# Kernel optimization log

Hardware: AMD Instinct MI355X
Metric: run time of the kernel (lower is better)

The kernel has to match this reference:

```python
import jax, jax.numpy as jnp
import numpy as np

B, S, E, H = 2, 2048, 1024, 16
DK = E // H


def setup_inputs() -> dict:
    key = jax.random.key(0)
    ks = jax.random.split(key, 8)
    scale = 1.0 / np.sqrt(E)
    inp = {
        "query": jax.random.normal(ks[0], (B, S, E), jnp.float32),
        "key": jax.random.normal(ks[1], (B, S, E), jnp.float32),
        "value": jax.random.normal(ks[2], (B, S, E), jnp.float32),
        # causal mask: True = masked out (upper triangle)
        "attn_mask": jnp.triu(jnp.ones((S, S), jnp.bool_), k=1),
        "Wq": jax.random.normal(ks[3], (E, E), jnp.float32) * scale,
        "bq": jnp.zeros((E,), jnp.float32),
        "Wk": jax.random.normal(ks[4], (E, E), jnp.float32) * scale,
        "bk": jnp.zeros((E,), jnp.float32),
        "Wv": jax.random.normal(ks[5], (E, E), jnp.float32) * scale,
        "bv": jnp.zeros((E,), jnp.float32),
        "Wo": jax.random.normal(ks[6], (E, E), jnp.float32) * scale,
        "bo": jnp.zeros((E,), jnp.float32),
    }
    return inp


def reference(query, key, value, attn_mask, Wq, bq, Wk, bk, Wv, bv, Wo, bo):
    bs = query.shape[0]
    # QKV projections, split heads: [B,S,E] -> [B,H,S,DK]
    def proj(x, W, b):
        y = jnp.einsum('bse,ef->bsf', x, W) + b
        return y.reshape(bs, -1, H, DK).transpose(0, 2, 1, 3)

    q = proj(query, Wq, bq)
    k = proj(key, Wk, bk)
    v = proj(value, Wv, bv)

    # scaled dot-product attention with additive -1e9 mask fill
    scores = jnp.einsum('bhqd,bhkd->bhqk', q, k) / np.sqrt(DK).astype(jnp.float32)
    scores = jnp.where(attn_mask[None, None, :, :], jnp.float32(-1e9), scores)
    attn = jax.nn.softmax(scores, axis=-1)
    ctx = jnp.einsum('bhqk,bhkd->bhqd', attn, v)  # [B,H,S,DK]

    concat = ctx.transpose(0, 2, 1, 3).reshape(bs, -1, E)  # [B,S,E]
    return jnp.einsum('bse,ef->bsf', concat, Wo) + bo
```

## Files before the change

kernel.cpp:

```cpp
#include <hip/hip_runtime.h>
#include <hip/hip_bf16.h>

typedef __attribute__((ext_vector_type(8))) short bf16x8;
typedef __attribute__((ext_vector_type(4))) float f32x4;

constexpr int Bc = 2, Sc = 2048, Ec = 1024, Hc = 16, DKc = 64;

__device__ __forceinline__ unsigned short f2b(float f) {
    union { float f; unsigned u; } v; v.f = f;
    unsigned u = v.u;
    return (unsigned short)((u + 0x7FFFu + ((u >> 16) & 1u)) >> 16);
}
__device__ __forceinline__ unsigned short f2bn(float f) {
    return __bfloat16_as_ushort(__float2bfloat16(f));
}
__device__ __forceinline__ float b2f(unsigned short h) {
    union { unsigned u; float f; } v; v.u = ((unsigned)h) << 16;
    return v.f;
}

#define GLOAD16(ldsp, gp)                                                                  \
    __builtin_amdgcn_global_load_lds((const __attribute__((address_space(1))) void*)(gp),  \
                                     (__attribute__((address_space(3))) void*)(ldsp),      \
                                     16, 0, 0)

#define ASM_VM4 asm volatile("s_waitcnt vmcnt(4)" ::: "memory")
#define ASM_VM0 asm volatile("s_waitcnt vmcnt(0)" ::: "memory")
#define ASM_LG0 asm volatile("s_waitcnt lgkmcnt(0)" ::: "memory")
#define ASM_BAR asm volatile("s_barrier" ::: "memory")

__global__ __launch_bounds__(256) void conv_x(
    const float* __restrict__ Xq, const float* __restrict__ Xk, const float* __restrict__ Xv,
    unsigned short* __restrict__ Xb)
{
    const int z = blockIdx.y;
    const float* X = (z == 0) ? Xq : (z == 1) ? Xk : Xv;
    unsigned short* O = Xb + (size_t)z * 4194304;
    const int n4 = 4194304 / 4;
    for (int i = blockIdx.x * 256 + threadIdx.x; i < n4; i += gridDim.x * 256) {
        float4 v = ((const float4*)X)[i];
        ushort4 h; h.x = f2b(v.x); h.y = f2b(v.y); h.z = f2b(v.z); h.w = f2b(v.w);
        ((ushort4*)O)[i] = h;
    }
}

__global__ __launch_bounds__(256) void conv_w(
    const float* __restrict__ Wq, const float* __restrict__ Wk,
    const float* __restrict__ Wv, const float* __restrict__ Wo,
    unsigned short* __restrict__ Wt)
{
    const int z = blockIdx.z;
    const float* W = (z == 0) ? Wq : (z == 1) ? Wk : (z == 2) ? Wv : Wo;
    unsigned short* O = Wt + (size_t)z * 1048576;
    __shared__ unsigned short T[64][65];
    const int k0 = blockIdx.y * 64, n0 = blockIdx.x * 64;
    const int tx = threadIdx.x & 15, ty = threadIdx.x >> 4;
    #pragma unroll
    for (int p = 0; p < 4; p++) {
        float4 v = *(const float4*)&W[(size_t)(k0 + ty + 16 * p) * 1024 + n0 + 4 * tx];
        T[ty + 16 * p][4 * tx + 0] = f2b(v.x);
        T[ty + 16 * p][4 * tx + 1] = f2b(v.y);
        T[ty + 16 * p][4 * tx + 2] = f2b(v.z);
        T[ty + 16 * p][4 * tx + 3] = f2b(v.w);
    }
    __syncthreads();
    #pragma unroll
    for (int p = 0; p < 4; p++) {
        ushort4 o;
        o.x = T[4 * tx + 0][ty + 16 * p];
        o.y = T[4 * tx + 1][ty + 16 * p];
        o.z = T[4 * tx + 2][ty + 16 * p];
        o.w = T[4 * tx + 3][ty + 16 * p];
        *(ushort4*)&O[(size_t)(n0 + ty + 16 * p) * 1024 + k0 + 4 * tx] = o;
    }
}

__global__ __launch_bounds__(512, 2) void gemm_qkv(
    const unsigned short* __restrict__ Xb, const unsigned short* __restrict__ Wt,
    const float* __restrict__ bq, const float* __restrict__ bk, const float* __restrict__ bv,
    unsigned short* __restrict__ Qw, unsigned short* __restrict__ Kw,
    unsigned short* __restrict__ Vt)
{
    const int wgid = blockIdx.x;
    const int xcd = wgid & 7;
    const int s = wgid >> 3;
    const int z = s >> 3;
    const int t8 = s & 7;
    const int nb = t8 >> 1;
    const int mb = (t8 & 1) * 8 + xcd;

    const unsigned short* Ag = Xb + (size_t)z * 4194304;
    const unsigned short* Bg = Wt + (size_t)z * 1048576;
    const float* bias = (z == 0) ? bq : (z == 1) ? bk : bv;

    __shared__ __align__(16) unsigned short SMEM[32768];

    const int tid = threadIdx.x;
    const int m0 = mb * 256, n0 = nb * 256;
    const int lane = tid & 63, c = lane & 15, g = lane >> 4;
    const int w = tid >> 6;
    const int wr = w >> 2;
    const int wc = w & 3;
    const int lcs = ((lane & 3) ^ ((lane >> 3) & 3)) * 8;
    const int rowin = (lane >> 2);

#define QKV_STAGE(buf, kk)                                                                 \
    _Pragma("unroll")                                                                      \
    for (int r2 = 0; r2 < 2; r2++) {                                                       \
        GLOAD16((char*)SMEM + (buf) * 16384 + r2 * 8192 + w * 1024,                        \
                Ag + (size_t)(m0 + r2 * 128 + w * 16 + rowin) * 1024 + (kk) + lcs);        \
        GLOAD16((char*)SMEM + 32768 + (buf) * 16384 + r2 * 8192 + w * 1024,                \
                Bg + (size_t)(n0 + r2 * 128 + w * 16 + rowin) * 1024 + (kk) + lcs);        \
    }

    f32x4 acc[8][4] = {};
    QKV_STAGE(0, 0)
    QKV_STAGE(1, 32)
    for (int t = 0; t < 32; t++) {
        const int cur = t & 1;
        if (t < 31) { ASM_VM4; } else { ASM_VM0; }
        ASM_BAR;
        bf16x8 a[8], b[4];
        const int rchk = (g ^ ((c >> 1) & 3)) << 4;
        #pragma unroll
        for (int m = 0; m < 8; m++)
            a[m] = *(const bf16x8*)((const char*)SMEM + cur * 16384 +
                                    (wr * 128 + m * 16 + c) * 64 + rchk);
        #pragma unroll
        for (int n = 0; n < 4; n++)
            b[n] = *(const bf16x8*)((const char*)SMEM + 32768 + cur * 16384 +
                                    (wc * 64 + n * 16 + c) * 64 + rchk);
        ASM_LG0;
        ASM_BAR;
        if (t + 2 < 32) { QKV_STAGE(cur, (t + 2) * 32) }
        __builtin_amdgcn_s_setprio(1);
        #pragma unroll
        for (int m = 0; m < 8; m++)
            #pragma unroll
            for (int n = 0; n < 4; n++)
                acc[m][n] = __builtin_amdgcn_mfma_f32_16x16x32_bf16(a[m], b[n], acc[m][n], 0, 0, 0);
        __builtin_amdgcn_s_setprio(0);
    }
#undef QKV_STAGE

    if (z == 2) {
        unsigned short* Tr = SMEM;
        #pragma unroll
        for (int p = 0; p < 2; p++) {
            ASM_BAR;
            if ((wc >> 1) == p) {
                #pragma unroll
                for (int n = 0; n < 4; n++) {
                    const int dl = (wc & 1) * 64 + n * 16 + c;
                    const float bv_ = bias[n0 + p * 128 + dl];
                    #pragma unroll
                    for (int m = 0; m < 8; m++) {
                        const int sl = wr * 128 + m * 16 + 4 * g;
                        ushort4 pw;
                        pw.x = f2bn(acc[m][n][0] + bv_);
                        pw.y = f2bn(acc[m][n][1] + bv_);
                        pw.z = f2bn(acc[m][n][2] + bv_);
                        pw.w = f2bn(acc[m][n][3] + bv_);
                        const int sc = (sl >> 2) ^ (dl & 7);
                        *(ushort4*)&Tr[dl * 256 + sc * 4] = pw;
                    }
                }
            }
            ASM_BAR;
            #pragma unroll
            for (int it = 0; it < 16; it++) {
                const int idx = it * 512 + tid;
                const int dl = idx >> 6;
                const int sc0 = idx & 63;
                const int sc = sc0 ^ (dl & 7);
                const ushort4 pw = *(const ushort4*)&Tr[dl * 256 + sc * 4];
                const int gn = n0 + p * 128 + dl;
                const int h = gn >> 6, d = gn & 63;
                const int gm = m0 + sc0 * 4;
                const int bb = gm >> 11, ss = gm & 2047;
                *(ushort4*)&Vt[((size_t)(bb * Hc + h) * DKc + d) * Sc + ss] = pw;
            }
        }
    } else {
        #pragma unroll
        for (int n = 0; n < 4; n++) {
            const int gn = n0 + wc * 64 + n * 16 + c;
            const float bv_ = bias[gn];
            const int h = gn >> 6, d = gn & 63;
            #pragma unroll
            for (int m = 0; m < 8; m++) {
                #pragma unroll
                for (int r = 0; r < 4; r++) {
                    const int gm = m0 + wr * 128 + m * 16 + 4 * g + r;
                    const int bb = gm >> 11, ss = gm & 2047;
                    const float val = acc[m][n][r] + bv_;
                    if (z == 0)
                        Qw[((size_t)(bb * Hc + h) * Sc + ss) * DKc + d] = f2bn(val * 0.125f);
                    else
                        Kw[((size_t)(bb * Hc + h) * Sc + ss) * DKc + d] = f2bn(val);
                }
            }
        }
    }
}

__global__ __launch_bounds__(256) void gemm_out(
    const unsigned short* __restrict__ Ctx, const unsigned short* __restrict__ Wt,
    const float* __restrict__ bo, float* __restrict__ Out)
{
    const int wgid = blockIdx.x;
    const int xcd = wgid & 7, slot = wgid >> 3;
    const int y = xcd + 8 * (slot & 3);
    const int x = slot >> 2;

    const unsigned short* Ag = Ctx;
    const unsigned short* Bg = Wt + (size_t)3 * 1048576;

    __shared__ __align__(16) unsigned short SMEM[4][4096];

    const int tid = threadIdx.x;
    const int m0 = y * 128, n0 = x * 128;
    const int lane = tid & 63, c = lane & 15, g = lane >> 4;
    const int w = tid >> 6;
    const int wr = (w >> 1) * 64, wc = (w & 1) * 64;
    const int lr = lane >> 2;
    const int lcs = ((lane & 3) ^ ((lane >> 3) & 3)) * 8;

#define OUT_STAGE(buf, kk)                                                                 \
    _Pragma("unroll")                                                                      \
    for (int i = 0; i < 2; i++) {                                                          \
        const int rb = 32 * w + 16 * i;                                                    \
        GLOAD16(SMEM[buf] + rb * 32, Ag + (size_t)(m0 + rb + lr) * 1024 + (kk) + lcs);     \
        GLOAD16(SMEM[2 + (buf)] + rb * 32, Bg + (size_t)(n0 + rb + lr) * 1024 + (kk) + lcs); \
    }

    f32x4 acc[4][4] = {};
    OUT_STAGE(0, 0)
    OUT_STAGE(1, 32)
    for (int t = 0; t < 32; t++) {
        const int cur = t & 1;
        if (t < 31) { ASM_VM4; } else { ASM_VM0; }
        ASM_BAR;
        bf16x8 a[4], b[4];
        #pragma unroll
        for (int m = 0; m < 4; m++)
            a[m] = *(const bf16x8*)((const char*)SMEM[cur] +
                   (wr + 16 * m + c) * 64 + ((g ^ ((c >> 1) & 3)) << 4));
        #pragma unroll
        for (int n = 0; n < 4; n++)
            b[n] = *(const bf16x8*)((const char*)SMEM[2 + cur] +
                   (wc + 16 * n + c) * 64 + ((g ^ ((c >> 1) & 3)) << 4));
        ASM_LG0;
        ASM_BAR;
        if (t + 2 < 32) { OUT_STAGE(cur, (t + 2) * 32) }
        __builtin_amdgcn_s_setprio(1);
        #pragma unroll
        for (int m = 0; m < 4; m++)
            #pragma unroll
            for (int n = 0; n < 4; n++)
                acc[m][n] = __builtin_amdgcn_mfma_f32_16x16x32_bf16(a[m], b[n], acc[m][n], 0, 0, 0);
        __builtin_amdgcn_s_setprio(0);
    }
#undef OUT_STAGE

    #pragma unroll
    for (int n = 0; n < 4; n++) {
        const int gn = n0 + wc + n * 16 + c;
        const float bv_ = bo[gn];
        #pragma unroll
        for (int m = 0; m < 4; m++) {
            #pragma unroll
            for (int r = 0; r < 4; r++) {
                const int gm = m0 + wr + m * 16 + 4 * g + r;
                Out[(size_t)gm * Ec + gn] = acc[m][n][r] + bv_;
            }
        }
    }
}

__global__ __launch_bounds__(256) void attn(
    const unsigned short* __restrict__ Qw, const unsigned short* __restrict__ Kw,
    const unsigned short* __restrict__ Vt,
    unsigned short* __restrict__ Opart, float* __restrict__ Lpart)
{
    const int bid = blockIdx.x;
    const int bh = bid & 31;
    const int ps = bid >> 5;
    const int pair = ps >> 1, sp = ps & 1;
    const int tid = threadIdx.x, w = tid >> 6, lane = tid & 63;
    const int c = lane & 15, g = lane >> 4;

    const unsigned short* Qh = Qw + (size_t)bh * Sc * DKc;
    const unsigned short* Kh = Kw + (size_t)bh * Sc * DKc;
    const unsigned short* Vh = Vt + (size_t)bh * DKc * Sc;

    __shared__ __align__(16) unsigned short Kl[4096];
    __shared__ __align__(16) unsigned short Vl[4096];
    __shared__ __align__(16) unsigned short Pl[4][16][72];

    const int lrow8 = lane >> 3;
    const int cbp = ((lane & 7) ^ lrow8) << 4;
    const int swz = (c & 7) << 4;

#define STAGE_KV(KV0)                                                                       \
    _Pragma("unroll")                                                                       \
    for (int s2 = 0; s2 < 2; s2++) {                                                        \
        const int row_ = s2 * 32 + w * 8 + lrow8;                                           \
        GLOAD16((char*)Kl + s2 * 4096 + w * 1024,                                           \
                (const char*)Kh + (size_t)((KV0) + row_) * 128 + cbp);                      \
        GLOAD16((char*)Vl + s2 * 4096 + w * 1024,                                           \
                (const char*)Vh + (size_t)row_ * 4096 + (size_t)(KV0) * 2 + cbp);           \
    }

    for (int half = 0; half < 2; half++) {
        const int qt = half ? (31 - pair) : pair;
        const int qbase = qt * 64;
        const int qrow = qbase + w * 16 + c;
        const int qtg = bh * 32 + qt;

        const bf16x8 q0 = *(const bf16x8*)&Qh[(size_t)qrow * DKc + 8 * g];
        const bf16x8 q1 = *(const bf16x8*)&Qh[(size_t)qrow * DKc + 32 + 8 * g];

        float lsum = 0.f;
        f32x4 o[4] = {};

        for (int j = sp; j <= qt; j += 2) {
            const int kv0 = j * 64;
            const bool maskt = (j == qt);

            STAGE_KV(kv0)
            __syncthreads();

            f32x4 d[4] = {};
            __builtin_amdgcn_s_setprio(1);
            #pragma unroll
            for (int t = 0; t < 4; t++) {
                const char* kb = (const char*)Kl + (16 * t + c) * 128;
                const bf16x8 k0 = *(const bf16x8*)(kb + ((16 * g) ^ swz));
                const bf16x8 k1 = *(const bf16x8*)(kb + ((64 + 16 * g) ^ swz));
                d[t] = __builtin_amdgcn_mfma_f32_16x16x32_bf16(k0, q0, d[t], 0, 0, 0);
                d[t] = __builtin_amdgcn_mfma_f32_16x16x32_bf16(k1, q1, d[t], 0, 0, 0);
            }
            __builtin_amdgcn_s_setprio(0);

            float s[16];
            if (maskt) {
                #pragma unroll
                for (int t = 0; t < 4; t++)
                    #pragma unroll
                    for (int r = 0; r < 4; r++) {
                        const int kv = kv0 + 16 * t + 4 * g + r;
                        s[4 * t + r] = __expf((kv <= qrow) ? d[t][r] : -1e30f);
                    }
            } else {
                #pragma unroll
                for (int t = 0; t < 4; t++)
                    #pragma unroll
                    for (int r = 0; r < 4; r++)
                        s[4 * t + r] = __expf(d[t][r]);
            }
            #pragma unroll
            for (int i = 0; i < 16; i++) lsum += s[i];

            #pragma unroll
            for (int t = 0; t < 4; t++) {
                ushort4 pw;
                pw.x = f2bn(s[4 * t + 0]); pw.y = f2bn(s[4 * t + 1]);
                pw.z = f2bn(s[4 * t + 2]); pw.w = f2bn(s[4 * t + 3]);
                *(ushort4*)&Pl[w][c][16 * t + 4 * g] = pw;
            }
            const bf16x8 pA0 = *(const bf16x8*)&Pl[w][c][8 * g];
            const bf16x8 pA1 = *(const bf16x8*)&Pl[w][c][32 + 8 * g];

            __builtin_amdgcn_s_setprio(1);
            #pragma unroll
            for (int ch = 0; ch < 4; ch++) {
                const char* vb = (const char*)Vl + (16 * ch + c) * 128;
                const bf16x8 v0 = *(const bf16x8*)(vb + ((16 * g) ^ swz));
                const bf16x8 v1 = *(const bf16x8*)(vb + ((64 + 16 * g) ^ swz));
                f32x4 t = o[ch];
                t = __builtin_amdgcn_mfma_f32_16x16x32_bf16(pA0, v0, t, 0, 0, 0);
                o[ch] = __builtin_amdgcn_mfma_f32_16x16x32_bf16(pA1, v1, t, 0, 0, 0);
            }
            __builtin_amdgcn_s_setprio(0);
            __syncthreads();
        }

        lsum += __shfl_xor(lsum, 16);
        lsum += __shfl_xor(lsum, 32);
        if (g == 0)
            Lpart[((size_t)sp * 1024 + qtg) * 64 + w * 16 + c] = lsum;

        #pragma unroll
        for (int ch = 0; ch < 4; ch++) {
            #pragma unroll
            for (int r = 0; r < 4; r++) {
                const int lrow = w * 16 + 4 * g + r;
                Opart[(((size_t)sp * 1024 + qtg) * 64 + lrow) * 64 + ch * 16 + c] =
                    f2bn(o[ch][r]);
            }
        }
    }
#undef STAGE_KV
}

__global__ __launch_bounds__(256) void attn_combine(
    const unsigned short* __restrict__ Opart, const float* __restrict__ Lpart,
    unsigned short* __restrict__ Ctx)
{
    const int qtg = blockIdx.x;
    const int bh = qtg >> 5, qt = qtg & 31;
    const int bb = bh >> 4, hh = bh & 15;
    #pragma unroll
    for (int it = 0; it < 2; it++) {
        const int chunk = threadIdx.x + it * 256;
        const int row = chunk >> 3, c8 = (chunk & 7) * 8;
        const size_t o0 = ((size_t)qtg * 64 + row) * 64 + c8;
        const size_t o1 = ((size_t)(1024 + qtg) * 64 + row) * 64 + c8;
        const bf16x8 a = *(const bf16x8*)&Opart[o0];
        const bf16x8 b = *(const bf16x8*)&Opart[o1];
        const float linv = 1.f / (Lpart[(size_t)qtg * 64 + row] +
                                  Lpart[(size_t)(1024 + qtg) * 64 + row]);
        ushort4 lo, hi;
        lo.x = f2bn((b2f((unsigned short)a[0]) + b2f((unsigned short)b[0])) * linv);
        lo.y = f2bn((b2f((unsigned short)a[1]) + b2f((unsigned short)b[1])) * linv);
        lo.z = f2bn((b2f((unsigned short)a[2]) + b2f((unsigned short)b[2])) * linv);
        lo.w = f2bn((b2f((unsigned short)a[3]) + b2f((unsigned short)b[3])) * linv);
        hi.x = f2bn((b2f((unsigned short)a[4]) + b2f((unsigned short)b[4])) * linv);
        hi.y = f2bn((b2f((unsigned short)a[5]) + b2f((unsigned short)b[5])) * linv);
        hi.z = f2bn((b2f((unsigned short)a[6]) + b2f((unsigned short)b[6])) * linv);
        hi.w = f2bn((b2f((unsigned short)a[7]) + b2f((unsigned short)b[7])) * linv);
        const int qg = qt * 64 + row;
        unsigned short* dst = &Ctx[((size_t)(bb * Sc + qg)) * Ec + hh * 64 + c8];
        *(ushort4*)dst = lo;
        *(ushort4*)(dst + 4) = hi;
    }
}

extern "C" void kernel_launch(void* const* d_in, const int* in_sizes, int n_in,
                              void* d_out, int out_size, void* d_ws, size_t ws_size,
                              hipStream_t stream) {
    const float* query = (const float*)d_in[0];
    const float* key   = (const float*)d_in[1];
    const float* value = (const float*)d_in[2];
    const float* Wq = (const float*)d_in[4];
    const float* bq = (const float*)d_in[5];
    const float* Wk = (const float*)d_in[6];
    const float* bk = (const float*)d_in[7];
    const float* Wv = (const float*)d_in[8];
    const float* bv = (const float*)d_in[9];
    const float* Wo = (const float*)d_in[10];
    const float* bo = (const float*)d_in[11];

    const size_t n_elem = (size_t)Bc * Hc * Sc * DKc;
    unsigned short* Qw = (unsigned short*)d_ws;
    unsigned short* Kw = Qw + n_elem;
    unsigned short* Vt = Kw + n_elem;
    unsigned short* Cx = Vt + n_elem;
    unsigned short* Xb = Cx + n_elem;
    unsigned short* Wt = Xb + 3 * n_elem;

    unsigned short* Opart = Xb;
    float* Lpart = (float*)(Xb + (size_t)2 * 1024 * 64 * 64);

    conv_x<<<dim3(512, 3), 256, 0, stream>>>(query, key, value, Xb);
    conv_w<<<dim3(16, 16, 4), 256, 0, stream>>>(Wq, Wk, Wv, Wo, Wt);
    gemm_qkv<<<dim3(192), 512, 0, stream>>>(Xb, Wt, bq, bk, bv, Qw, Kw, Vt);
    attn<<<dim3(1024), 256, 0, stream>>>(Qw, Kw, Vt, Opart, Lpart);
    attn_combine<<<dim3(1024), 256, 0, stream>>>(Opart, Lpart, Cx);
    gemm_out<<<dim3(256), 256, 0, stream>>>(Cx, Wt, bo, (float*)d_out);
}
```

Baseline: 107.8 us.

## Retile QKV GEMM to 256x128 tiles with 4 waves and split-phase MFMA pipeline

The QKV projection GEMM moves from 256x256 tiles on 512 threads to 256x128 tiles on 256 threads, launching 384 workgroups instead of 192. The mainloop is restructured: the next K-slice is prefetched at the top of each iteration, and the A fragments are loaded and consumed in two halves separated by barriers and sched fences. The XCD-aware block mapping is replaced with a plain modulo mapping. This aims for better CU occupancy and load balance on 256 CUs and lower register pressure, at the cost of more redundant A-tile loads and more barriers per iteration.

New measurement: 111.8 us. 3.8% more time.

```diff
diff --git a/kernel.cpp b/kernel.cpp
--- a/kernel.cpp
+++ b/kernel.cpp
@@ -28,6 +28,7 @@
 #define ASM_VM0 asm volatile("s_waitcnt vmcnt(0)" ::: "memory")
 #define ASM_LG0 asm volatile("s_waitcnt lgkmcnt(0)" ::: "memory")
 #define ASM_BAR asm volatile("s_barrier" ::: "memory")
+#define SCHED_FENCE __builtin_amdgcn_sched_barrier(0)
 
 __global__ __launch_bounds__(256) void conv_x(
     const float* __restrict__ Xq, const float* __restrict__ Xk, const float* __restrict__ Xv,
@@ -75,87 +76,98 @@
     }
 }
 
-__global__ __launch_bounds__(512, 2) void gemm_qkv(
+__global__ __launch_bounds__(256, 2) void gemm_qkv(
     const unsigned short* __restrict__ Xb, const unsigned short* __restrict__ Wt,
     const float* __restrict__ bq, const float* __restrict__ bk, const float* __restrict__ bv,
     unsigned short* __restrict__ Qw, unsigned short* __restrict__ Kw,
     unsigned short* __restrict__ Vt)
 {
     const int wgid = blockIdx.x;
-    const int xcd = wgid & 7;
-    const int s = wgid >> 3;
-    const int z = s >> 3;
-    const int t8 = s & 7;
-    const int nb = t8 >> 1;
-    const int mb = (t8 & 1) * 8 + xcd;
+    const int zm = wgid % 48, nb = wgid / 48;
+    const int z = zm >> 4, mb = zm & 15;
 
     const unsigned short* Ag = Xb + (size_t)z * 4194304;
     const unsigned short* Bg = Wt + (size_t)z * 1048576;
     const float* bias = (z == 0) ? bq : (z == 1) ? bk : bv;
 
-    __shared__ __align__(16) unsigned short SMEM[32768];
+    __shared__ __align__(16) unsigned short SA[2][8192];
+    __shared__ __align__(16) unsigned short SB[2][4096];
 
     const int tid = threadIdx.x;
-    const int m0 = mb * 256, n0 = nb * 256;
+    const int m0 = mb * 256, n0 = nb * 128;
     const int lane = tid & 63, c = lane & 15, g = lane >> 4;
     const int w = tid >> 6;
-    const int wr = w >> 2;
-    const int wc = w & 3;
+    const int wrh = w >> 1;
+    const int wnh = w & 1;
+    const int lr = lane >> 2;
     const int lcs = ((lane & 3) ^ ((lane >> 3) & 3)) * 8;
-    const int rowin = (lane >> 2);
-
-#define QKV_STAGE(buf, kk)                                                                 \
+
+#define QKV_STAGE(dbuf, kt)                                                                \
     _Pragma("unroll")                                                                      \
-    for (int r2 = 0; r2 < 2; r2++) {                                                       \
-        GLOAD16((char*)SMEM + (buf) * 16384 + r2 * 8192 + w * 1024,                        \
-                Ag + (size_t)(m0 + r2 * 128 + w * 16 + rowin) * 1024 + (kk) + lcs);        \
-        GLOAD16((char*)SMEM + 32768 + (buf) * 16384 + r2 * 8192 + w * 1024,                \
-                Bg + (size_t)(n0 + r2 * 128 + w * 16 + rowin) * 1024 + (kk) + lcs);        \
-    }
+    for (int i = 0; i < 4; i++)                                                            \
+        GLOAD16((char*)SA[dbuf] + i * 4096 + w * 1024,                                     \
+                Ag + (size_t)(m0 + i * 64 + w * 16 + lr) * 1024 + (kt) * 32 + lcs);        \
+    _Pragma("unroll")                                                                      \
+    for (int i = 0; i < 2; i++)                                                            \
+        GLOAD16((char*)SB[dbuf] + i * 4096 + w * 1024,                                     \
+                Bg + (size_t)(n0 + i * 64 + w * 16 + lr) * 1024 + (kt) * 32 + lcs);
 
     f32x4 acc[8][4] = {};
+    const int slot = (g ^ ((c >> 1) & 3)) << 4;
+
     QKV_STAGE(0, 0)
-    QKV_STAGE(1, 32)
+    ASM_VM0; ASM_BAR;
+
     for (int t = 0; t < 32; t++) {
-        const int cur = t & 1;
-        if (t < 31) { ASM_VM4; } else { ASM_VM0; }
-        ASM_BAR;
-        bf16x8 a[8], b[4];
-        const int rchk = (g ^ ((c >> 1) & 3)) << 4;
-        #pragma unroll
-        for (int m = 0; m < 8; m++)
-            a[m] = *(const bf16x8*)((const char*)SMEM + cur * 16384 +
-                                    (wr * 128 + m * 16 + c) * 64 + rchk);
+        const int d = t & 1;
+        if (t + 1 < 32) { QKV_STAGE(d ^ 1, t + 1) }
+        bf16x8 aR[4], bR[4];
+        #pragma unroll
+        for (int m = 0; m < 4; m++)
+            aR[m] = *(const bf16x8*)((const char*)SA[d] + (wrh * 128 + m * 16 + c) * 64 + slot);
         #pragma unroll
         for (int n = 0; n < 4; n++)
-            b[n] = *(const bf16x8*)((const char*)SMEM + 32768 + cur * 16384 +
-                                    (wc * 64 + n * 16 + c) * 64 + rchk);
-        ASM_LG0;
-        ASM_BAR;
-        if (t + 2 < 32) { QKV_STAGE(cur, (t + 2) * 32) }
+            bR[n] = *(const bf16x8*)((const char*)SB[d] + (wnh * 64 + n * 16 + c) * 64 + slot);
+        ASM_BAR;
+        ASM_LG0; SCHED_FENCE;
         __builtin_amdgcn_s_setprio(1);
         #pragma unroll
-        for (int m = 0; m < 8; m++)
+        for (int m = 0; m < 4; m++)
             #pragma unroll
             for (int n = 0; n < 4; n++)
-                acc[m][n] = __builtin_amdgcn_mfma_f32_16x16x32_bf16(a[m], b[n], acc[m][n], 0, 0, 0);
+                acc[m][n] = __builtin_amdgcn_mfma_f32_16x16x32_bf16(aR[m], bR[n], acc[m][n], 0, 0, 0);
         __builtin_amdgcn_s_setprio(0);
+        ASM_BAR;
+        #pragma unroll
+        for (int m = 0; m < 4; m++)
+            aR[m] = *(const bf16x8*)((const char*)SA[d] + (wrh * 128 + (m + 4) * 16 + c) * 64 + slot);
+        ASM_BAR;
+        ASM_LG0; SCHED_FENCE;
+        __builtin_amdgcn_s_setprio(1);
+        #pragma unroll
+        for (int m = 0; m < 4; m++)
+            #pragma unroll
+            for (int n = 0; n < 4; n++)
+                acc[m + 4][n] = __builtin_amdgcn_mfma_f32_16x16x32_bf16(aR[m], bR[n], acc[m + 4][n], 0, 0, 0);
+        __builtin_amdgcn_s_setprio(0);
+        ASM_VM0;
+        ASM_BAR;
     }
 #undef QKV_STAGE
 
     if (z == 2) {
-        unsigned short* Tr = SMEM;
+        unsigned short* Tr = &SA[0][0];
         #pragma unroll
         for (int p = 0; p < 2; p++) {
             ASM_BAR;
-            if ((wc >> 1) == p) {
+            if (wnh == p) {
                 #pragma unroll
                 for (int n = 0; n < 4; n++) {
-                    const int dl = (wc & 1) * 64 + n * 16 + c;
-                    const float bv_ = bias[n0 + p * 128 + dl];
+                    const int dl = n * 16 + c;
+                    const float bv_ = bias[n0 + p * 64 + dl];
                     #pragma unroll
                     for (int m = 0; m < 8; m++) {
-                        const int sl = wr * 128 + m * 16 + 4 * g;
+                        const int sl = wrh * 128 + m * 16 + 4 * g;
                         ushort4 pw;
                         pw.x = f2bn(acc[m][n][0] + bv_);
                         pw.y = f2bn(acc[m][n][1] + bv_);
@@ -169,35 +181,35 @@
             ASM_BAR;
             #pragma unroll
             for (int it = 0; it < 16; it++) {
-                const int idx = it * 512 + tid;
+                const int idx = it * 256 + tid;
                 const int dl = idx >> 6;
                 const int sc0 = idx & 63;
                 const int sc = sc0 ^ (dl & 7);
                 const ushort4 pw = *(const ushort4*)&Tr[dl * 256 + sc * 4];
-                const int gn = n0 + p * 128 + dl;
-                const int h = gn >> 6, d = gn & 63;
+                const int gn = n0 + p * 64 + dl;
+                const int h = gn >> 6, dd = gn & 63;
                 const int gm = m0 + sc0 * 4;
                 const int bb = gm >> 11, ss = gm & 2047;
-                *(ushort4*)&Vt[((size_t)(bb * Hc + h) * DKc + d) * Sc + ss] = pw;
+                *(ushort4*)&Vt[((size_t)(bb * Hc + h) * DKc + dd) * Sc + ss] = pw;
             }
         }
     } else {
         #pragma unroll
         for (int n = 0; n < 4; n++) {
-            const int gn = n0 + wc * 64 + n * 16 + c;
+            const int gn = n0 + wnh * 64 + n * 16 + c;
             const float bv_ = bias[gn];
-            const int h = gn >> 6, d = gn & 63;
+            const int h = gn >> 6, dd = gn & 63;
             #pragma unroll
             for (int m = 0; m < 8; m++) {
                 #pragma unroll
                 for (int r = 0; r < 4; r++) {
-                    const int gm = m0 + wr * 128 + m * 16 + 4 * g + r;
+                    const int gm = m0 + wrh * 128 + m * 16 + 4 * g + r;
                     const int bb = gm >> 11, ss = gm & 2047;
                     const float val = acc[m][n][r] + bv_;
                     if (z == 0)
-                        Qw[((size_t)(bb * Hc + h) * Sc + ss) * DKc + d] = f2bn(val * 0.125f);
+                        Qw[((size_t)(bb * Hc + h) * Sc + ss) * DKc + dd] = f2bn(val * 0.125f);
                     else
-                        Kw[((size_t)(bb * Hc + h) * Sc + ss) * DKc + d] = f2bn(val);
+                        Kw[((size_t)(bb * Hc + h) * Sc + ss) * DKc + dd] = f2bn(val);
                 }
             }
         }
@@ -465,7 +477,7 @@
 
     conv_x<<<dim3(512, 3), 256, 0, stream>>>(query, key, value, Xb);
     conv_w<<<dim3(16, 16, 4), 256, 0, stream>>>(Wq, Wk, Wv, Wo, Wt);
-    gemm_qkv<<<dim3(192), 512, 0, stream>>>(Xb, Wt, bq, bk, bv, Qw, Kw, Vt);
+    gemm_qkv<<<dim3(384), 256, 0, stream>>>(Xb, Wt, bq, bk, bv, Qw, Kw, Vt);
     attn<<<dim3(1024), 256, 0, stream>>>(Qw, Kw, Vt, Opart, Lpart);
     attn_combine<<<dim3(1024), 256, 0, stream>>>(Opart, Lpart, Cx);
     gemm_out<<<dim3(256), 256, 0, stream>>>(Cx, Wt, bo, (float*)d_out);
```
